# Optimization experiments

Hardware: AMD Instinct MI355X
Metric: run time of the kernel (lower is better)

## Reference

```python
import jax, jax.numpy as jnp
import numpy as np

K = 4      # number of per-slot Linear layers (self.k)
H = 512    # hidden_dim
B = 4      # branching factor at every tree level (B >= K -> no padded slots)
T = 1024   # number of trees (roots)
D = 3      # pooled tree levels (= idx_matrix.shape[1] - 2)
N0 = T * B ** D  # 65536 leaves


def _make_level(n_in):
    """Replicates the torch order_matrix / pooling construction for groups of size B.
    order[m, i] = group_base + (pos_in_group + m) % B, then +1 for the zero pad row.
    seg[i] = group id (torch.repeat_interleave of counts)."""
    i = np.arange(n_in)
    base = (i // B) * B
    pos = i % B
    m = np.arange(K)[:, None]
    order = base[None, :] + (pos[None, :] + m) % B + 1  # [K, n_in], all valid since B >= K
    seg = i // B
    return order.astype(np.int32), seg.astype(np.int32)


def setup_inputs() -> dict:
    key = jax.random.key(0)
    ks = jax.random.split(key, 5)
    x = jax.random.normal(ks[0], (N0, H), jnp.float32)
    node_idx = jnp.arange(N0, dtype=jnp.int32)  # idx_matrix[:, -1]
    o1, s1 = _make_level(N0)
    o2, s2 = _make_level(N0 // B)
    o3, s3 = _make_level(N0 // B // B)
    Wz = jax.random.normal(ks[1], (K, H, H), jnp.float32) / np.sqrt(H)   # k slot Linears
    bz = jax.random.normal(ks[2], (K, H), jnp.float32) * 0.02
    Wzf = jax.random.normal(ks[3], (H, H), jnp.float32) / np.sqrt(H)     # z_final_layer
    bzf = jax.random.normal(ks[4], (H,), jnp.float32) * 0.02
    return dict(x=x, Wz=Wz, bz=bz, Wzf=Wzf, bzf=bzf, node_idx=node_idx,
                order1=jnp.asarray(o1), order2=jnp.asarray(o2), order3=jnp.asarray(o3),
                seg1=jnp.asarray(s1), seg2=jnp.asarray(s2), seg3=jnp.asarray(s3))


def _tree_layer(data, order, seg, num_seg, Wz, bz, Wzf, bzf):
    # prepend zero row so padded entries (order == 0) gather zeros
    padded = jnp.concatenate([jnp.zeros((1, data.shape[-1]), data.dtype), data], axis=0)
    emb = padded[order]                                    # [K, N, H] gather
    emb = jnp.einsum('knh,kjh->nkj', emb, Wz) + bz[None]   # per-slot Linear (x @ W.T + b)
    emb = jnp.where((order.T == 0)[..., None], jnp.zeros((), emb.dtype), emb)  # mask padded slots
    emb = emb.sum(axis=1)                                  # sum over K slots -> [N, H]
    emb = emb @ Wzf.T + bzf                                # z_final_layer
    return jax.ops.segment_sum(emb, seg, num_segments=num_seg)  # global_add_pool


def reference(x, Wz, bz, Wzf, bzf, node_idx, order1, order2, order3, seg1, seg2, seg3):
    data = x[node_idx]
    for order, seg in ((order1, seg1), (order2, seg2), (order3, seg3)):
        data = _tree_layer(data, order, seg, order.shape[1] // B, Wz, bz, Wzf, bzf)
    return data  # [T, H]
```

## Files before the change

### kernel.cpp

```cpp
#include <hip/hip_runtime.h>


#define HD 512

typedef __attribute__((ext_vector_type(8))) short bf16x8;
typedef __attribute__((ext_vector_type(4))) float f32x4;

struct __align__(16) MfmaSmem {
    unsigned short Ah[64][40];
    unsigned short Al[64][40];
    unsigned short Bh[64][40];
    unsigned short Bl[64][40];
};

__device__ __forceinline__ void split8(const float4& v0, const float4& v1,
                                       bf16x8& hv, bf16x8& lv) {
    float f[8] = {v0.x, v0.y, v0.z, v0.w, v1.x, v1.y, v1.z, v1.w};
    #pragma unroll
    for (int i = 0; i < 8; ++i) {
        unsigned u = __float_as_uint(f[i]);
        hv[i] = (short)(u >> 16);
        float hi = __uint_as_float(u & 0xFFFF0000u);
        lv[i] = (short)(__float_as_uint(f[i] - hi) >> 16);
    }
}

template<bool BIAS>
__device__ __forceinline__
void mfma_gemm(const float* __restrict__ A, const float* __restrict__ Bt,
               float* __restrict__ C, const float* __restrict__ bias,
               float bscale, int i0, int j0, MfmaSmem& sm) {
    const int t = threadIdx.x;
    const int sr = t >> 2, sk = (t & 3) << 3;
    const int lane = t & 63, w = t >> 6;
    const int fm = lane & 15, fq = (lane >> 4) << 3;

    const float* ap = &A[(size_t)(i0 + sr) * HD + sk];
    const float* bp = &Bt[(size_t)(j0 + sr) * HD + sk];
    float4 a0 = *(const float4*)ap,      a1 = *(const float4*)(ap + 4);
    float4 b0 = *(const float4*)bp,      b1 = *(const float4*)(bp + 4);

    f32x4 acc[4] = {};

    for (int it = 0; it < 16; ++it) {
        __syncthreads();
        bf16x8 hv, lv;
        split8(a0, a1, hv, lv);
        *(bf16x8*)&sm.Ah[sr][sk] = hv;
        *(bf16x8*)&sm.Al[sr][sk] = lv;
        split8(b0, b1, hv, lv);
        *(bf16x8*)&sm.Bh[sr][sk] = hv;
        *(bf16x8*)&sm.Bl[sr][sk] = lv;
        __syncthreads();

        if (it < 15) {
            const int k0n = (it + 1) << 5;
            a0 = *(const float4*)(ap + k0n);
            a1 = *(const float4*)(ap + k0n + 4);
            b0 = *(const float4*)(bp + k0n);
            b1 = *(const float4*)(bp + k0n + 4);
        }

        bf16x8 ah = *(const bf16x8*)&sm.Ah[(w << 4) + fm][fq];
        bf16x8 al = *(const bf16x8*)&sm.Al[(w << 4) + fm][fq];
        #pragma unroll
        for (int ct = 0; ct < 4; ++ct) {
            bf16x8 bh = *(const bf16x8*)&sm.Bh[(ct << 4) + fm][fq];
            bf16x8 bl = *(const bf16x8*)&sm.Bl[(ct << 4) + fm][fq];
            acc[ct] = __builtin_amdgcn_mfma_f32_16x16x32_bf16(ah, bh, acc[ct], 0, 0, 0);
            acc[ct] = __builtin_amdgcn_mfma_f32_16x16x32_bf16(ah, bl, acc[ct], 0, 0, 0);
            acc[ct] = __builtin_amdgcn_mfma_f32_16x16x32_bf16(al, bh, acc[ct], 0, 0, 0);
        }
    }

    const int orow = i0 + (w << 4) + ((lane >> 4) << 2);
    #pragma unroll
    for (int ct = 0; ct < 4; ++ct) {
        const int col = j0 + (ct << 4) + fm;
        float bv = BIAS ? bscale * bias[col] : 0.f;
        #pragma unroll
        for (int r = 0; r < 4; ++r)
            C[(size_t)(orow + r) * HD + col] = acc[ct][r] + bv;
    }
}

union D1Smem {
    float  tp[64][68];
    float4 red[128];
};

__global__ __launch_bounds__(256) void kD1(
        const float* __restrict__ x, const float* __restrict__ Wz,
        const float* __restrict__ bz, const float* __restrict__ Wzf,
        const float* __restrict__ bzf,
        float* __restrict__ part, float* __restrict__ WsumT, float* __restrict__ c0) {
    __shared__ D1Smem sm;
    const int b = blockIdx.x, t = threadIdx.x;
    if (b < 2048) {
        const int tree = b >> 1, half = b & 1;
        const int c = t & 127, sub = t >> 7;
        const float4* xp = (const float4*)x + (size_t)tree * 8192
                         + (half * 32 + sub * 16) * 128 + c;
        float4 acc = make_float4(0.f, 0.f, 0.f, 0.f);
        #pragma unroll
        for (int g = 0; g < 2; ++g) {
            float4 v[8];
            #pragma unroll
            for (int i = 0; i < 8; ++i) v[i] = xp[(size_t)(g * 8 + i) * 128];
            #pragma unroll
            for (int i = 0; i < 8; ++i) {
                acc.x += v[i].x; acc.y += v[i].y; acc.z += v[i].z; acc.w += v[i].w;
            }
        }
        if (sub) sm.red[c] = acc;
        __syncthreads();
        if (!sub) {
            float4 o = sm.red[c];
            acc.x += o.x; acc.y += o.y; acc.z += o.z; acc.w += o.w;
            ((float4*)part)[b * 128 + c] = acc;
        }
    } else if (b < 2112) {
        const int bb = b - 2048;
        const int j0t = (bb >> 3) << 6, h0t = (bb & 7) << 6;
        const int rr = t >> 4, cc = (t & 15) << 2;
        #pragma unroll
        for (int p = 0; p < 4; ++p) {
            const float* wp = &Wz[(size_t)(j0t + rr + 16 * p) * HD + h0t + cc];
            float4 s = *(const float4*)wp;
            #pragma unroll
            for (int q = 1; q < 4; ++q) {
                float4 v = *(const float4*)(wp + q * 262144);
                s.x += v.x; s.y += v.y; s.z += v.z; s.w += v.w;
            }
            *(float4*)&sm.tp[rr + 16 * p][cc] = s;
        }
        __syncthreads();
        #pragma unroll
        for (int p = 0; p < 4; ++p) {
            const int hr = rr + 16 * p;
            float4 o = make_float4(sm.tp[cc + 0][hr], sm.tp[cc + 1][hr],
                                   sm.tp[cc + 2][hr], sm.tp[cc + 3][hr]);
            *(float4*)&WsumT[(size_t)(h0t + hr) * HD + j0t + cc] = o;
        }
    } else {
        const int lane = t & 63, w = t >> 6, hb = lane << 3;
        const int j = (b - 2112) * 4 + w;
        float4 s0 = *(const float4*)&bz[hb];
        float4 s1 = *(const float4*)&bz[hb + 4];
        #pragma unroll
        for (int q = 1; q < 4; ++q) {
            float4 t0 = *(const float4*)&bz[q * HD + hb];
            float4 t1 = *(const float4*)&bz[q * HD + hb + 4];
            s0.x += t0.x; s0.y += t0.y; s0.z += t0.z; s0.w += t0.w;
            s1.x += t1.x; s1.y += t1.y; s1.z += t1.z; s1.w += t1.w;
        }
        const float4* wr = (const float4*)&Wzf[(size_t)j * HD + hb];
        float4 w0 = wr[0], w1 = wr[1];
        float p = w0.x * s0.x + w0.y * s0.y + w0.z * s0.z + w0.w * s0.w
                + w1.x * s1.x + w1.y * s1.y + w1.z * s1.z + w1.w * s1.w;
        #pragma unroll
        for (int off = 32; off > 0; off >>= 1) p += __shfl_down(p, off);
        if (lane == 0) c0[j] = 4.f * (p + bzf[j]);
    }
}

__global__ __launch_bounds__(256) void kD2(
        const float* __restrict__ Wzf, const float* __restrict__ WsumT,
        const float* __restrict__ part,
        float* __restrict__ M, float* __restrict__ MT, float* __restrict__ P3) {
    __shared__ MfmaSmem sm;
    const int b = blockIdx.x, t = threadIdx.x;
    if (b < 64) {
        mfma_gemm<false>(Wzf, WsumT, M, nullptr, 0.f,
                         (b >> 3) << 6, (b & 7) << 6, sm);
    } else if (b < 128) {
        const int bb = b - 64;
        mfma_gemm<false>(WsumT, Wzf, MT, nullptr, 0.f,
                         (bb >> 3) << 6, (bb & 7) << 6, sm);
    } else {
        const int gid = (b - 128) * 256 + t;
        const float4* p4 = (const float4*)part;
        float4* o4 = (float4*)P3;
        #pragma unroll
        for (int h = 0; h < 2; ++h) {
            const int i = gid + h * 65536;
            const int tree = i >> 7, c = i & 127;
            float4 pa = p4[(size_t)(2 * tree) * 128 + c];
            float4 pb = p4[(size_t)(2 * tree + 1) * 128 + c];
            pa.x += pb.x; pa.y += pb.y; pa.z += pb.z; pa.w += pb.w;
            o4[i] = pa;
        }
    }
}

__global__ __launch_bounds__(256) void kD3(
        const float* __restrict__ P3, const float* __restrict__ M,
        const float* __restrict__ MT, const float* __restrict__ c0,
        float* __restrict__ Y1, float* __restrict__ M2, float* __restrict__ u) {
    __shared__ MfmaSmem sm;
    const int b = blockIdx.x, t = threadIdx.x;
    if (b < 128) {
        mfma_gemm<true>(P3, M, Y1, c0, 16.f, (b >> 3) << 6, (b & 7) << 6, sm);
    } else if (b < 192) {
        const int bb = b - 128;
        mfma_gemm<false>(M, MT, M2, nullptr, 0.f,
                         (bb >> 3) << 6, (bb & 7) << 6, sm);
    } else {
        const int lane = t & 63, w = t >> 6, hb = lane << 3;
        const int j = (b - 192) * 4 + w;
        const float4* mr = (const float4*)&M[(size_t)j * HD + hb];
        const float4* cr = (const float4*)&c0[hb];
        float4 m0 = mr[0], m1 = mr[1], q0 = cr[0], q1 = cr[1];
        float p = m0.x * q0.x + m0.y * q0.y + m0.z * q0.z + m0.w * q0.w
                + m1.x * q1.x + m1.y * q1.y + m1.z * q1.z + m1.w * q1.w;
        #pragma unroll
        for (int off = 32; off > 0; off >>= 1) p += __shfl_down(p, off);
        if (lane == 0) u[j] = 4.f * p + c0[j];
    }
}

__global__ __launch_bounds__(256) void kD4(
        const float* __restrict__ Y1, const float* __restrict__ M2,
        const float* __restrict__ u, float* __restrict__ out) {
    __shared__ MfmaSmem sm;
    const int b = blockIdx.x;
    mfma_gemm<true>(Y1, M2, out, u, 1.f, (b >> 3) << 6, (b & 7) << 6, sm);
}

extern "C" void kernel_launch(void* const* d_in, const int* in_sizes, int n_in,
                              void* d_out, int out_size, void* d_ws, size_t ws_size,
                              hipStream_t stream) {
    const float* x   = (const float*)d_in[0];
    const float* Wz  = (const float*)d_in[1];
    const float* bz  = (const float*)d_in[2];
    const float* Wzf = (const float*)d_in[3];
    const float* bzf = (const float*)d_in[4];
    float* out = (float*)d_out;

    float* ws    = (float*)d_ws;
    float* P3    = ws;
    float* Y1    = ws + 524288;
    float* WsumT = ws + 1048576;
    float* M     = ws + 1310720;
    float* MT    = ws + 1572864;
    float* M2    = ws + 1835008;
    float* part  = ws + 2097152;
    float* c0    = ws + 3145728;
    float* u     = ws + 3146240;

    hipLaunchKernelGGL(kD1, dim3(2240), dim3(256), 0, stream,
                       x, Wz, bz, Wzf, bzf, part, WsumT, c0);
    hipLaunchKernelGGL(kD2, dim3(384), dim3(256), 0, stream,
                       Wzf, WsumT, part, M, MT, P3);
    hipLaunchKernelGGL(kD3, dim3(320), dim3(256), 0, stream,
                       P3, M, MT, c0, Y1, M2, u);
    hipLaunchKernelGGL(kD4, dim3(128), dim3(256), 0, stream, Y1, M2, u, out);
}
```

Baseline: 254.1 us.

## Fuse Wz-sum and M/MT GEMMs into first kernel, drop one launch

Computes M = Wzf·ΣWz and its transpose with a scalar FP32 tiled GEMM inside the first kernel, summing the four Wz slices on the fly instead of materialising WsumT. The per-tree leaf reduction now writes P3 directly, with each block handling half the columns over all 64 leaves rather than a partial that a later kernel combines. This removes one kernel launch, the WsumT and partial-sum round trips through global memory, and one dependent stage. In exchange, the 512×512 GEMMs move from split-bf16 MFMA to scalar FMA and reread Wz four times per tile.

```diff
diff --git a/kernel.cpp b/kernel.cpp
--- a/kernel.cpp
+++ b/kernel.cpp
@@ -37,8 +37,8 @@
 
     const float* ap = &A[(size_t)(i0 + sr) * HD + sk];
     const float* bp = &Bt[(size_t)(j0 + sr) * HD + sk];
-    float4 a0 = *(const float4*)ap,      a1 = *(const float4*)(ap + 4);
-    float4 b0 = *(const float4*)bp,      b1 = *(const float4*)(bp + 4);
+    float4 a0 = *(const float4*)ap, a1 = *(const float4*)(ap + 4);
+    float4 b0 = *(const float4*)bp, b1 = *(const float4*)(bp + 4);
 
     f32x4 acc[4] = {};
 
@@ -84,23 +84,72 @@
     }
 }
 
-union D1Smem {
-    float  tp[64][68];
-    float4 red[128];
-};
+struct VSmem { float As[16][33]; float Bs[16][33]; };
+
+template<int MODE>
+__device__ __forceinline__
+void vgemm(const float* __restrict__ Wzf, const float* __restrict__ Wz,
+           float* __restrict__ C, int i0, int j0, VSmem& sm) {
+    const int t = threadIdx.x;
+    const int ti = t >> 4, tj = t & 15;
+    float a00 = 0.f, a01 = 0.f, a10 = 0.f, a11 = 0.f;
+
+    for (int k0 = 0; k0 < HD; k0 += 16) {
+        __syncthreads();
+        {
+            const int r = t >> 3, kp = (t & 7) << 1;
+            const int row = (MODE == 0) ? i0 + r : j0 + r;
+            float2 v = *(const float2*)&Wzf[(size_t)row * HD + k0 + kp];
+            if (MODE == 0) { sm.As[kp][r] = v.x; sm.As[kp + 1][r] = v.y; }
+            else           { sm.Bs[kp][r] = v.x; sm.Bs[kp + 1][r] = v.y; }
+        }
+        {
+            const int kk = t >> 4, j2 = (t & 15) << 1;
+            const int col = (MODE == 0) ? j0 + j2 : i0 + j2;
+            const float* src = &Wz[(size_t)(k0 + kk) * HD + col];
+            float sx = 0.f, sy = 0.f;
+            #pragma unroll
+            for (int q = 0; q < 4; ++q) {
+                float2 v = *(const float2*)(src + q * 262144);
+                sx += v.x; sy += v.y;
+            }
+            if (MODE == 0) { sm.Bs[kk][j2] = sx; sm.Bs[kk][j2 + 1] = sy; }
+            else           { sm.As[kk][j2] = sx; sm.As[kk][j2 + 1] = sy; }
+        }
+        __syncthreads();
+        #pragma unroll
+        for (int kk = 0; kk < 16; ++kk) {
+            float x0 = sm.As[kk][2 * ti], x1 = sm.As[kk][2 * ti + 1];
+            float y0 = sm.Bs[kk][2 * tj], y1 = sm.Bs[kk][2 * tj + 1];
+            a00 = fmaf(x0, y0, a00); a01 = fmaf(x0, y1, a01);
+            a10 = fmaf(x1, y0, a10); a11 = fmaf(x1, y1, a11);
+        }
+    }
+    float* c0p = &C[(size_t)(i0 + 2 * ti) * HD + j0 + 2 * tj];
+    c0p[0] = a00; c0p[1] = a01;
+    c0p[HD] = a10; c0p[HD + 1] = a11;
+}
+
+union D1Smem { VSmem v; float4 red[192]; };
 
 __global__ __launch_bounds__(256) void kD1(
         const float* __restrict__ x, const float* __restrict__ Wz,
         const float* __restrict__ bz, const float* __restrict__ Wzf,
         const float* __restrict__ bzf,
-        float* __restrict__ part, float* __restrict__ WsumT, float* __restrict__ c0) {
+        float* __restrict__ P3, float* __restrict__ M, float* __restrict__ MT,
+        float* __restrict__ c0) {
     __shared__ D1Smem sm;
     const int b = blockIdx.x, t = threadIdx.x;
-    if (b < 2048) {
-        const int tree = b >> 1, half = b & 1;
-        const int c = t & 127, sub = t >> 7;
+    if (b < 256) {
+        vgemm<0>(Wzf, Wz, M, (b >> 4) << 5, (b & 15) << 5, sm.v);
+    } else if (b < 512) {
+        const int bb = b - 256;
+        vgemm<1>(Wzf, Wz, MT, (bb >> 4) << 5, (bb & 15) << 5, sm.v);
+    } else if (b < 2560) {
+        const int pb = b - 512, tree = pb >> 1, cbase = (pb & 1) << 6;
+        const int c = t & 63, sub = t >> 6;
         const float4* xp = (const float4*)x + (size_t)tree * 8192
-                         + (half * 32 + sub * 16) * 128 + c;
+                         + (sub << 4) * 128 + cbase + c;
         float4 acc = make_float4(0.f, 0.f, 0.f, 0.f);
         #pragma unroll
         for (int g = 0; g < 2; ++g) {
@@ -112,39 +161,19 @@
                 acc.x += v[i].x; acc.y += v[i].y; acc.z += v[i].z; acc.w += v[i].w;
             }
         }
-        if (sub) sm.red[c] = acc;
+        if (sub) sm.red[((sub - 1) << 6) + c] = acc;
         __syncthreads();
         if (!sub) {
-            float4 o = sm.red[c];
-            acc.x += o.x; acc.y += o.y; acc.z += o.z; acc.w += o.w;
-            ((float4*)part)[b * 128 + c] = acc;
-        }
-    } else if (b < 2112) {
-        const int bb = b - 2048;
-        const int j0t = (bb >> 3) << 6, h0t = (bb & 7) << 6;
-        const int rr = t >> 4, cc = (t & 15) << 2;
-        #pragma unroll
-        for (int p = 0; p < 4; ++p) {
-            const float* wp = &Wz[(size_t)(j0t + rr + 16 * p) * HD + h0t + cc];
-            float4 s = *(const float4*)wp;
-            #pragma unroll
-            for (int q = 1; q < 4; ++q) {
-                float4 v = *(const float4*)(wp + q * 262144);
-                s.x += v.x; s.y += v.y; s.z += v.z; s.w += v.w;
-            }
-            *(float4*)&sm.tp[rr + 16 * p][cc] = s;
-        }
-        __syncthreads();
-        #pragma unroll
-        for (int p = 0; p < 4; ++p) {
-            const int hr = rr + 16 * p;
-            float4 o = make_float4(sm.tp[cc + 0][hr], sm.tp[cc + 1][hr],
-                                   sm.tp[cc + 2][hr], sm.tp[cc + 3][hr]);
-            *(float4*)&WsumT[(size_t)(h0t + hr) * HD + j0t + cc] = o;
+            float4 r0 = sm.red[c], r1 = sm.red[64 + c], r2 = sm.red[128 + c];
+            acc.x += (r0.x + r1.x) + r2.x;
+            acc.y += (r0.y + r1.y) + r2.y;
+            acc.z += (r0.z + r1.z) + r2.z;
+            acc.w += (r0.w + r1.w) + r2.w;
+            ((float4*)P3)[tree * 128 + cbase + c] = acc;
         }
     } else {
         const int lane = t & 63, w = t >> 6, hb = lane << 3;
-        const int j = (b - 2112) * 4 + w;
+        const int j = (b - 2560) * 4 + w;
         float4 s0 = *(const float4*)&bz[hb];
         float4 s1 = *(const float4*)&bz[hb + 4];
         #pragma unroll
@@ -165,35 +194,6 @@
 }
 
 __global__ __launch_bounds__(256) void kD2(
-        const float* __restrict__ Wzf, const float* __restrict__ WsumT,
-        const float* __restrict__ part,
-        float* __restrict__ M, float* __restrict__ MT, float* __restrict__ P3) {
-    __shared__ MfmaSmem sm;
-    const int b = blockIdx.x, t = threadIdx.x;
-    if (b < 64) {
-        mfma_gemm<false>(Wzf, WsumT, M, nullptr, 0.f,
-                         (b >> 3) << 6, (b & 7) << 6, sm);
-    } else if (b < 128) {
-        const int bb = b - 64;
-        mfma_gemm<false>(WsumT, Wzf, MT, nullptr, 0.f,
-                         (bb >> 3) << 6, (bb & 7) << 6, sm);
-    } else {
-        const int gid = (b - 128) * 256 + t;
-        const float4* p4 = (const float4*)part;
-        float4* o4 = (float4*)P3;
-        #pragma unroll
-        for (int h = 0; h < 2; ++h) {
-            const int i = gid + h * 65536;
-            const int tree = i >> 7, c = i & 127;
-            float4 pa = p4[(size_t)(2 * tree) * 128 + c];
-            float4 pb = p4[(size_t)(2 * tree + 1) * 128 + c];
-            pa.x += pb.x; pa.y += pb.y; pa.z += pb.z; pa.w += pb.w;
-            o4[i] = pa;
-        }
-    }
-}
-
-__global__ __launch_bounds__(256) void kD3(
         const float* __restrict__ P3, const float* __restrict__ M,
         const float* __restrict__ MT, const float* __restrict__ c0,
         float* __restrict__ Y1, float* __restrict__ M2, float* __restrict__ u) {
@@ -219,7 +219,7 @@
     }
 }
 
-__global__ __launch_bounds__(256) void kD4(
+__global__ __launch_bounds__(256) void kD3(
         const float* __restrict__ Y1, const float* __restrict__ M2,
         const float* __restrict__ u, float* __restrict__ out) {
     __shared__ MfmaSmem sm;
@@ -237,22 +237,18 @@
     const float* bzf = (const float*)d_in[4];
     float* out = (float*)d_out;
 
-    float* ws    = (float*)d_ws;
-    float* P3    = ws;
-    float* Y1    = ws + 524288;
-    float* WsumT = ws + 1048576;
-    float* M     = ws + 1310720;
-    float* MT    = ws + 1572864;
-    float* M2    = ws + 1835008;
-    float* part  = ws + 2097152;
-    float* c0    = ws + 3145728;
-    float* u     = ws + 3146240;
-
-    hipLaunchKernelGGL(kD1, dim3(2240), dim3(256), 0, stream,
-                       x, Wz, bz, Wzf, bzf, part, WsumT, c0);
-    hipLaunchKernelGGL(kD2, dim3(384), dim3(256), 0, stream,
-                       Wzf, WsumT, part, M, MT, P3);
-    hipLaunchKernelGGL(kD3, dim3(320), dim3(256), 0, stream,
+    float* ws = (float*)d_ws;
+    float* P3 = ws;
+    float* Y1 = ws + 524288;
+    float* M  = ws + 1048576;
+    float* MT = ws + 1310720;
+    float* M2 = ws + 1572864;
+    float* c0 = ws + 1835008;
+    float* u  = ws + 1835520;
+
+    hipLaunchKernelGGL(kD1, dim3(2688), dim3(256), 0, stream,
+                       x, Wz, bz, Wzf, bzf, P3, M, MT, c0);
+    hipLaunchKernelGGL(kD2, dim3(320), dim3(256), 0, stream,
                        P3, M, MT, c0, Y1, M2, u);
-    hipLaunchKernelGGL(kD4, dim3(128), dim3(256), 0, stream, Y1, M2, u, out);
-}
+    hipLaunchKernelGGL(kD3, dim3(128), dim3(256), 0, stream, Y1, M2, u, out);
+}
```

Result: no change. 254.2 us (+0.1%).
